# Kernel tuning notes

Measured on AMD Instinct MI355X. Metric: run time of the kernel, lower is better.

Reference implementation:

```python
import jax, jax.numpy as jnp
import numpy as np

B, A, C, H, S, NR = 128, 2048, 128, 512, 3, 2
PR = C + 3 + S   # 134 read params per head
PW = 3 * C + 3 + S  # 390 write params


def setup_inputs() -> dict:
    key = jax.random.key(0)
    ks = jax.random.split(key, 8)
    h = jax.random.normal(ks[0], (B, H), jnp.float32)
    mem = jax.random.normal(ks[1], (B, A, C), jnp.float32)
    ra = jax.random.uniform(ks[2], (NR, B, A), jnp.float32)
    ra = ra / ra.sum(-1, keepdims=True)  # valid attention distributions
    wa = jax.random.uniform(ks[3], (B, A), jnp.float32)
    wa = wa / wa.sum(-1, keepdims=True)
    W_read = 0.02 * jax.random.normal(ks[4], (NR, PR, H), jnp.float32)
    b_read = jnp.zeros((NR, PR), jnp.float32)
    W_write = 0.02 * jax.random.normal(ks[5], (PW, H), jnp.float32)
    b_write = jnp.zeros((PW,), jnp.float32)
    return dict(h=h, mem=mem, prev_read_attn=ra, prev_write_attn=wa,
                W_read=W_read, b_read=b_read, W_write=W_write, b_write=b_write)


def _addressing(query, beta, gate, shift, gamma, mem, prev_w):
    """NTM addressing. query [...,C] (raw), beta/gate/gamma [...,1], shift [...,S],
    mem [B,A,C] (broadcasts), prev_w [...,A]. Returns attention [...,A]."""
    eps = 1e-8
    q = jax.nn.sigmoid(query)
    beta = jax.nn.softplus(beta) + 1.0
    gate = jax.nn.sigmoid(gate)
    shift_w = jax.nn.softmax(shift, axis=-1)
    gamma = jax.nn.softplus(gamma) + 1.0
    # content-based addressing: cosine similarity + sharpened softmax over A
    qn = jnp.maximum(jnp.linalg.norm(q, axis=-1, keepdims=True), eps)      # [...,1]
    mn = jnp.maximum(jnp.linalg.norm(mem, axis=-1), eps)                   # [B,A]
    sim = jnp.einsum('...c,...ac->...a', q, mem) / (qn * mn)
    w_c = jax.nn.softmax(beta * sim, axis=-1)
    # gated interpolation with previous attention
    w_g = gate * w_c + (1.0 - gate) * prev_w
    # circular shift convolution, offsets -(S//2)..S//2
    K = S // 2
    idx = (jnp.arange(A)[:, None] - (jnp.arange(S)[None, :] - K)) % A      # [A,S]
    w_s = jnp.einsum('...as,...s->...a', w_g[..., idx], shift_w)
    # gamma sharpening
    w_pow = w_s ** gamma
    return w_pow / (w_pow.sum(-1, keepdims=True) + 1e-12)


def reference(h, mem, prev_read_attn, prev_write_attn, W_read, b_read, W_write, b_write):
    # --- read heads (vectorized over NR heads) ---
    pr = jnp.einsum('bh,rph->rbp', h, W_read) + b_read[:, None, :]         # [NR,B,PR]
    q, beta, gate, shift, gamma = jnp.split(pr, [C, C + 1, C + 2, C + 2 + S], axis=-1)
    read_w = _addressing(q, beta, gate, shift, gamma, mem, prev_read_attn)  # [NR,B,A]
    read_vectors = jnp.einsum('rba,bac->rbc', read_w, mem)                 # [NR,B,C]
    # --- write head ---
    pw = h @ W_write.T + b_write                                           # [B,PW]
    locs = np.cumsum([C, 1, 1, S, 1, C])
    qw, bw, gw, sw, gmw, erase, add = jnp.split(pw, locs.tolist(), axis=-1)
    write_w = _addressing(qw, bw, gw, sw, gmw, mem, prev_write_attn)       # [B,A]
    e = jax.nn.sigmoid(erase)[:, None, :]                                  # [B,1,C]
    a = jax.nn.sigmoid(add)[:, None, :]                                    # [B,1,C]
    w = write_w[..., None]                                                 # [B,A,1]
    new_mem = mem * (1.0 - w * e) + w * a
    return read_vectors, new_mem
```

## Files before the change

### kernel.cpp

```cpp
#include <hip/hip_runtime.h>
#include <math.h>

constexpr int B_  = 128;
constexpr int A_  = 2048;
constexpr int C_  = 128;
constexpr int H_  = 512;
constexpr int S_  = 3;
constexpr int NR_ = 2;
constexpr int PR_ = C_ + 3 + S_;
constexpr int PW_ = 3 * C_ + 3 + S_;

typedef float vfloat4 __attribute__((ext_vector_type(4)));

__device__ __forceinline__ float sigmoidf_(float x) { return 1.0f / (1.0f + expf(-x)); }
__device__ __forceinline__ float softplusf_(float x) {
  return fmaxf(x, 0.0f) + log1pf(expf(-fabsf(x)));
}

__device__ __forceinline__ float waveReduceSum(float v) {
#pragma unroll
  for (int off = 32; off; off >>= 1) v += __shfl_xor(v, off, 64);
  return v;
}
__device__ __forceinline__ float waveReduceMax(float v) {
#pragma unroll
  for (int off = 32; off; off >>= 1) v = fmaxf(v, __shfl_xor(v, off, 64));
  return v;
}

__device__ __forceinline__ float blockReduceSum(float v, float* rbuf) {
  int tid = threadIdx.x;
  v = waveReduceSum(v);
  if ((tid & 63) == 0) rbuf[tid >> 6] = v;
  __syncthreads();
  float r = rbuf[0] + rbuf[1] + rbuf[2] + rbuf[3];
  __syncthreads();
  return r;
}
__device__ __forceinline__ float blockReduceMax(float v, float* rbuf) {
  int tid = threadIdx.x;
  v = waveReduceMax(v);
  if ((tid & 63) == 0) rbuf[tid >> 6] = v;
  __syncthreads();
  float r = fmaxf(fmaxf(rbuf[0], rbuf[1]), fmaxf(rbuf[2], rbuf[3]));
  __syncthreads();
  return r;
}

__global__ __launch_bounds__(256) void proj_kernel(
    const float* __restrict__ h, const float* __restrict__ Wr,
    const float* __restrict__ br, const float* __restrict__ Ww,
    const float* __restrict__ bw, float* __restrict__ pr, float* __restrict__ pw) {
  constexpr int NPR = NR_ * B_ * PR_;
  constexpr int NPW = B_ * PW_;
  int wave = (blockIdx.x * blockDim.x + threadIdx.x) >> 6;
  int lane = threadIdx.x & 63;
  const float* wrow;
  const float* hrow;
  float bias;
  float* outp;
  if (wave < NPR) {
    int r = wave / (B_ * PR_);
    int rem = wave - r * (B_ * PR_);
    int b = rem / PR_;
    int p = rem - b * PR_;
    wrow = Wr + (size_t)(r * PR_ + p) * H_;
    hrow = h + (size_t)b * H_;
    bias = br[r * PR_ + p];
    outp = pr + wave;
  } else {
    int w2 = wave - NPR;
    if (w2 >= NPW) return;
    int b = w2 / PW_;
    int p = w2 - b * PW_;
    wrow = Ww + (size_t)p * H_;
    hrow = h + (size_t)b * H_;
    bias = bw[p];
    outp = pw + w2;
  }
  const float4* w4 = (const float4*)wrow;
  const float4* h4 = (const float4*)hrow;
  float4 a0 = h4[(lane << 1)];
  float4 a1 = h4[(lane << 1) + 1];
  float4 b0 = w4[(lane << 1)];
  float4 b1 = w4[(lane << 1) + 1];
  float acc = a0.x * b0.x;
  acc = fmaf(a0.y, b0.y, acc);
  acc = fmaf(a0.z, b0.z, acc);
  acc = fmaf(a0.w, b0.w, acc);
  acc = fmaf(a1.x, b1.x, acc);
  acc = fmaf(a1.y, b1.y, acc);
  acc = fmaf(a1.z, b1.z, acc);
  acc = fmaf(a1.w, b1.w, acc);
  acc = waveReduceSum(acc);
  if (lane == 0) *outp = acc + bias;
}

__global__ __launch_bounds__(64) void headprep_kernel(
    const float* __restrict__ pr, const float* __restrict__ pw,
    float* __restrict__ qbuf, float* __restrict__ qn, float* __restrict__ pars,
    float* __restrict__ rv) {
  int hb = blockIdx.x;
  int hd = hb >> 7;
  int b = hb & (B_ - 1);
  int lane = threadIdx.x;
  for (int i = hb * 64 + lane; i < NR_ * B_ * C_; i += 384 * 64) rv[i] = 0.0f;

  const float* src = (hd < 2) ? (pr + (size_t)hb * PR_) : (pw + (size_t)b * PW_);
  float2 raw = ((const float2*)src)[lane];
  float q0 = sigmoidf_(raw.x);
  float q1 = sigmoidf_(raw.y);
  ((float2*)(qbuf + (size_t)hb * C_))[lane] = make_float2(q0, q1);
  float ss = q0 * q0 + q1 * q1;
  ss = waveReduceSum(ss);
  if (lane == 0) {
    qn[hb] = fmaxf(sqrtf(ss), 1e-8f);
    float braw = src[C_];
    float graw = src[C_ + 1];
    float s0 = src[C_ + 2], s1 = src[C_ + 3], s2 = src[C_ + 4];
    float gmraw = src[C_ + 5];
    float mx = fmaxf(s0, fmaxf(s1, s2));
    float e0 = expf(s0 - mx), e1 = expf(s1 - mx), e2 = expf(s2 - mx);
    float inv = 1.0f / (e0 + e1 + e2);
    float* pp = pars + hb * 8;
    pp[0] = softplusf_(braw) + 1.0f;
    pp[1] = sigmoidf_(graw);
    pp[2] = e0 * inv;
    pp[3] = e1 * inv;
    pp[4] = e2 * inv;
    pp[5] = softplusf_(gmraw) + 1.0f;
  }
}

__global__ __launch_bounds__(256) void sim_kernel(
    const float* __restrict__ mem, const float* __restrict__ qbuf,
    const float* __restrict__ qn, float* __restrict__ sim) {
  __shared__ __align__(16) float qs[3 * C_];
  __shared__ float qnl[3];
  int b = blockIdx.x >> 5;
  int chunk = blockIdx.x & 31;
  int rowbase = chunk << 6;
  int tid = threadIdx.x;
  for (int idx = tid; idx < 3 * C_; idx += 256) {
    int hd = idx >> 7;
    int c = idx & (C_ - 1);
    qs[idx] = qbuf[(size_t)(hd * B_ + b) * C_ + c];
  }
  if (tid < 3) qnl[tid] = qn[tid * B_ + b];
  __syncthreads();

  int wv = tid >> 6;
  int lane = tid & 63;
  int j = lane & 7;
  int rsub = lane >> 3;

  float4 q0[4], q1[4], q2[4];
  const float4* qs4 = (const float4*)qs;
#pragma unroll
  for (int k = 0; k < 4; k++) {
    q0[k] = qs4[j + 8 * k];
    q1[k] = qs4[32 + j + 8 * k];
    q2[k] = qs4[64 + j + 8 * k];
  }
  float iqn0 = 1.0f / qnl[0], iqn1 = 1.0f / qnl[1], iqn2 = 1.0f / qnl[2];

#pragma unroll
  for (int it = 0; it < 2; it++) {
    int row = rowbase + (it << 5) + (wv << 3) + rsub;
    const float4* mrow = (const float4*)(mem + ((size_t)b * A_ + row) * C_);
    float d0 = 0.f, d1 = 0.f, d2 = 0.f, ss = 0.f;
#pragma unroll
    for (int k = 0; k < 4; k++) {
      float4 m = mrow[j + 8 * k];
      d0 = fmaf(m.x, q0[k].x, d0); d0 = fmaf(m.y, q0[k].y, d0);
      d0 = fmaf(m.z, q0[k].z, d0); d0 = fmaf(m.w, q0[k].w, d0);
      d1 = fmaf(m.x, q1[k].x, d1); d1 = fmaf(m.y, q1[k].y, d1);
      d1 = fmaf(m.z, q1[k].z, d1); d1 = fmaf(m.w, q1[k].w, d1);
      d2 = fmaf(m.x, q2[k].x, d2); d2 = fmaf(m.y, q2[k].y, d2);
      d2 = fmaf(m.z, q2[k].z, d2); d2 = fmaf(m.w, q2[k].w, d2);
      ss = fmaf(m.x, m.x, ss); ss = fmaf(m.y, m.y, ss);
      ss = fmaf(m.z, m.z, ss); ss = fmaf(m.w, m.w, ss);
    }
#pragma unroll
    for (int off = 1; off <= 4; off <<= 1) {
      d0 += __shfl_xor(d0, off, 64);
      d1 += __shfl_xor(d1, off, 64);
      d2 += __shfl_xor(d2, off, 64);
      ss += __shfl_xor(ss, off, 64);
    }
    if (j == 0) {
      float imn = 1.0f / fmaxf(sqrtf(ss), 1e-8f);
      sim[(size_t)(0 * B_ + b) * A_ + row] = d0 * iqn0 * imn;
      sim[(size_t)(1 * B_ + b) * A_ + row] = d1 * iqn1 * imn;
      sim[(size_t)(2 * B_ + b) * A_ + row] = d2 * iqn2 * imn;
    }
  }
}

__global__ __launch_bounds__(256) void attn_kernel(
    const float* __restrict__ sim, const float* __restrict__ ra,
    const float* __restrict__ wa, const float* __restrict__ pars,
    float* __restrict__ attn) {
  __shared__ float wg[A_];
  __shared__ float rbuf[4];
  int hb = blockIdx.x;
  int hd = hb >> 7;
  int b = hb & (B_ - 1);
  int tid = threadIdx.x;
  const float* pp = pars + hb * 8;
  float beta = pp[0], gate = pp[1], sw0 = pp[2], sw1 = pp[3], sw2 = pp[4], gamma = pp[5];
  const float* simrow = sim + (size_t)hb * A_;
  const float* prev = (hd < 2) ? (ra + (size_t)hb * A_) : (wa + (size_t)b * A_);
  float* outrow = attn + (size_t)hb * A_;

  float s[8];
  float mx = -1e30f;
#pragma unroll
  for (int i = 0; i < 8; i++) {
    s[i] = simrow[tid + (i << 8)];
    mx = fmaxf(mx, s[i]);
  }
  mx = blockReduceMax(mx, rbuf);
  float p[8];
  float lsum = 0.0f;
#pragma unroll
  for (int i = 0; i < 8; i++) {
    p[i] = expf(beta * (s[i] - mx));
    lsum += p[i];
  }
  float tot = blockReduceSum(lsum, rbuf);
  float inv = 1.0f / tot;
#pragma unroll
  for (int i = 0; i < 8; i++) {
    int a = tid + (i << 8);
    wg[a] = fmaf(gate, p[i] * inv, (1.0f - gate) * prev[a]);
  }
  __syncthreads();
  float lsum2 = 0.0f;
#pragma unroll
  for (int i = 0; i < 8; i++) {
    int a = tid + (i << 8);
    float ws = sw0 * wg[(a + 1) & (A_ - 1)] + sw1 * wg[a] + sw2 * wg[(a - 1) & (A_ - 1)];
    float wp = (ws > 0.0f) ? exp2f(gamma * log2f(ws)) : 0.0f;
    p[i] = wp;
    lsum2 += wp;
  }
  float tot2 = blockReduceSum(lsum2, rbuf);
  float inv2 = 1.0f / (tot2 + 1e-12f);
#pragma unroll
  for (int i = 0; i < 8; i++) {
    outrow[tid + (i << 8)] = p[i] * inv2;
  }
}

__global__ __launch_bounds__(256) void update_kernel(
    const float* __restrict__ mem, const float* __restrict__ attn,
    const float* __restrict__ pw, float* __restrict__ rv,
    float* __restrict__ nmem) {
  __shared__ float att0[256], att1[256], attw[256];
  __shared__ float4 red0[256];
  __shared__ float4 red1[256];
  int b = blockIdx.x >> 3;
  int chunk = blockIdx.x & 7;
  int rowbase = chunk << 8;
  int tid = threadIdx.x;
  att0[tid] = attn[(size_t)(0 * B_ + b) * A_ + rowbase + tid];
  att1[tid] = attn[(size_t)(1 * B_ + b) * A_ + rowbase + tid];
  attw[tid] = attn[(size_t)(2 * B_ + b) * A_ + rowbase + tid];
  __syncthreads();

  int rowlane = tid & 31;
  int rowoff = tid >> 5;
  int c0 = rowlane << 2;
  const float* pwrow = pw + (size_t)b * PW_;
  float2 eA = *(const float2*)(pwrow + C_ + 6 + c0);
  float2 eB = *(const float2*)(pwrow + C_ + 6 + c0 + 2);
  float2 aA = *(const float2*)(pwrow + 2 * C_ + 6 + c0);
  float2 aB = *(const float2*)(pwrow + 2 * C_ + 6 + c0 + 2);
  float e0 = sigmoidf_(eA.x), e1 = sigmoidf_(eA.y), e2 = sigmoidf_(eB.x), e3 = sigmoidf_(eB.y);
  float ad0 = sigmoidf_(aA.x), ad1 = sigmoidf_(aA.y), ad2 = sigmoidf_(aB.x), ad3 = sigmoidf_(aB.y);

  float4 acc0 = make_float4(0.f, 0.f, 0.f, 0.f);
  float4 acc1 = make_float4(0.f, 0.f, 0.f, 0.f);

#pragma unroll 4
  for (int i = 0; i < 32; i++) {
    int ridx = (i << 3) + rowoff;
    int row = rowbase + ridx;
    size_t base = ((size_t)b * A_ + row) * C_ + c0;
    float4 m = *(const float4*)(mem + base);
    float w0 = att0[ridx];
    float w1 = att1[ridx];
    float ww = attw[ridx];
    acc0.x = fmaf(w0, m.x, acc0.x);
    acc0.y = fmaf(w0, m.y, acc0.y);
    acc0.z = fmaf(w0, m.z, acc0.z);
    acc0.w = fmaf(w0, m.w, acc0.w);
    acc1.x = fmaf(w1, m.x, acc1.x);
    acc1.y = fmaf(w1, m.y, acc1.y);
    acc1.z = fmaf(w1, m.z, acc1.z);
    acc1.w = fmaf(w1, m.w, acc1.w);
    vfloat4 nm;
    nm.x = fmaf(m.x, 1.0f - ww * e0, ww * ad0);
    nm.y = fmaf(m.y, 1.0f - ww * e1, ww * ad1);
    nm.z = fmaf(m.z, 1.0f - ww * e2, ww * ad2);
    nm.w = fmaf(m.w, 1.0f - ww * e3, ww * ad3);
    __builtin_nontemporal_store(nm, (vfloat4*)(nmem + base));
  }

  red0[tid] = acc0;
  red1[tid] = acc1;
  __syncthreads();
#pragma unroll
  for (int s = 128; s >= 32; s >>= 1) {
    if (tid < s) {
      float4 x = red0[tid], y = red0[tid + s];
      x.x += y.x; x.y += y.y; x.z += y.z; x.w += y.w;
      red0[tid] = x;
      float4 u = red1[tid], v = red1[tid + s];
      u.x += v.x; u.y += v.y; u.z += v.z; u.w += v.w;
      red1[tid] = u;
    }
    __syncthreads();
  }
  if (tid < 32) {
    float4 r0 = red0[tid];
    float4 r1 = red1[tid];
    float* rv0 = rv + (size_t)(0 * B_ + b) * C_ + (tid << 2);
    float* rv1 = rv + (size_t)(1 * B_ + b) * C_ + (tid << 2);
    atomicAdd(rv0 + 0, r0.x);
    atomicAdd(rv0 + 1, r0.y);
    atomicAdd(rv0 + 2, r0.z);
    atomicAdd(rv0 + 3, r0.w);
    atomicAdd(rv1 + 0, r1.x);
    atomicAdd(rv1 + 1, r1.y);
    atomicAdd(rv1 + 2, r1.z);
    atomicAdd(rv1 + 3, r1.w);
  }
}

extern "C" void kernel_launch(void* const* d_in, const int* in_sizes, int n_in,
                              void* d_out, int out_size, void* d_ws, size_t ws_size,
                              hipStream_t stream) {
  const float* h   = (const float*)d_in[0];
  const float* mem = (const float*)d_in[1];
  const float* ra  = (const float*)d_in[2];
  const float* wa  = (const float*)d_in[3];
  const float* Wr  = (const float*)d_in[4];
  const float* br  = (const float*)d_in[5];
  const float* Ww  = (const float*)d_in[6];
  const float* bw  = (const float*)d_in[7];

  float* out = (float*)d_out;
  float* rv = out;
  float* nmem = out + NR_ * B_ * C_;

  float* ws = (float*)d_ws;
  float* pr_buf = ws;
  float* pw_buf = pr_buf + NR_ * B_ * PR_;
  float* qbuf   = pw_buf + B_ * PW_;
  float* qn     = qbuf + 3 * B_ * C_;
  float* pars   = qn + 3 * B_;
  float* simb   = pars + 3 * B_ * 8;

  constexpr int NWAVES = NR_ * B_ * PR_ + B_ * PW_;
  proj_kernel<<<dim3((NWAVES + 3) / 4), dim3(256), 0, stream>>>(h, Wr, br, Ww, bw, pr_buf, pw_buf);
  headprep_kernel<<<dim3(3 * B_), dim3(64), 0, stream>>>(pr_buf, pw_buf, qbuf, qn, pars, rv);
  sim_kernel<<<dim3(B_ * (A_ / 64)), dim3(256), 0, stream>>>(mem, qbuf, qn, simb);
  attn_kernel<<<dim3(3 * B_), dim3(256), 0, stream>>>(simb, ra, wa, pars, simb);
  update_kernel<<<dim3(B_ * (A_ / 256)), dim3(256), 0, stream>>>(mem, simb, pw_buf, rv, nmem);
}
```

Measured before the change: 291.3 us.

## Fold headprep into neighbors, pair projection rows, widen attn blocks, shuffle reductions

Removes the headprep kernel. Its sigmoid/norm work moves into sim_kernel, its scalar parameter transforms move into attn_kernel, and rv zeroing moves into proj_kernel. proj_kernel computes two outputs per wave so the h row load is shared. attn_kernel uses 1024-thread blocks with fewer reduction rounds, and update_kernel replaces the LDS tree reduction with a shuffle followed by a small LDS sum. The intent is to cut one launch and some sync overhead. The cost is that every sim block recomputes the sigmoid of q, and the pairing assumes the output counts are even and that row pairs stay within one head.

```diff
diff --git a/kernel.cpp b/kernel.cpp
--- a/kernel.cpp
+++ b/kernel.cpp
@@ -28,115 +28,84 @@
   return v;
 }
 
-__device__ __forceinline__ float blockReduceSum(float v, float* rbuf) {
-  int tid = threadIdx.x;
-  v = waveReduceSum(v);
-  if ((tid & 63) == 0) rbuf[tid >> 6] = v;
-  __syncthreads();
-  float r = rbuf[0] + rbuf[1] + rbuf[2] + rbuf[3];
-  __syncthreads();
-  return r;
-}
-__device__ __forceinline__ float blockReduceMax(float v, float* rbuf) {
-  int tid = threadIdx.x;
-  v = waveReduceMax(v);
-  if ((tid & 63) == 0) rbuf[tid >> 6] = v;
-  __syncthreads();
-  float r = fmaxf(fmaxf(rbuf[0], rbuf[1]), fmaxf(rbuf[2], rbuf[3]));
-  __syncthreads();
-  return r;
-}
-
 __global__ __launch_bounds__(256) void proj_kernel(
     const float* __restrict__ h, const float* __restrict__ Wr,
     const float* __restrict__ br, const float* __restrict__ Ww,
-    const float* __restrict__ bw, float* __restrict__ pr, float* __restrict__ pw) {
+    const float* __restrict__ bw, float* __restrict__ pr, float* __restrict__ pw,
+    float* __restrict__ rv) {
   constexpr int NPR = NR_ * B_ * PR_;
   constexpr int NPW = B_ * PW_;
-  int wave = (blockIdx.x * blockDim.x + threadIdx.x) >> 6;
+  int gid = blockIdx.x * 256 + threadIdx.x;
+  if (gid < NR_ * B_ * C_) rv[gid] = 0.0f;
+  int wave = gid >> 6;
   int lane = threadIdx.x & 63;
-  const float* wrow;
+  int out0 = wave * 2;
+  const float* w0row;
+  const float* w1row;
   const float* hrow;
-  float bias;
+  float bias0, bias1;
   float* outp;
-  if (wave < NPR) {
-    int r = wave / (B_ * PR_);
-    int rem = wave - r * (B_ * PR_);
+  if (out0 < NPR) {
+    int r = out0 / (B_ * PR_);
+    int rem = out0 - r * (B_ * PR_);
     int b = rem / PR_;
     int p = rem - b * PR_;
-    wrow = Wr + (size_t)(r * PR_ + p) * H_;
+    w0row = Wr + (size_t)(r * PR_ + p) * H_;
+    w1row = w0row + H_;
     hrow = h + (size_t)b * H_;
-    bias = br[r * PR_ + p];
-    outp = pr + wave;
+    bias0 = br[r * PR_ + p];
+    bias1 = br[r * PR_ + p + 1];
+    outp = pr + out0;
   } else {
-    int w2 = wave - NPR;
+    int w2 = out0 - NPR;
     if (w2 >= NPW) return;
     int b = w2 / PW_;
     int p = w2 - b * PW_;
-    wrow = Ww + (size_t)p * H_;
+    w0row = Ww + (size_t)p * H_;
+    w1row = w0row + H_;
     hrow = h + (size_t)b * H_;
-    bias = bw[p];
+    bias0 = bw[p];
+    bias1 = bw[p + 1];
     outp = pw + w2;
   }
-  const float4* w4 = (const float4*)wrow;
   const float4* h4 = (const float4*)hrow;
+  const float4* wa4 = (const float4*)w0row;
+  const float4* wb4 = (const float4*)w1row;
   float4 a0 = h4[(lane << 1)];
   float4 a1 = h4[(lane << 1) + 1];
-  float4 b0 = w4[(lane << 1)];
-  float4 b1 = w4[(lane << 1) + 1];
-  float acc = a0.x * b0.x;
-  acc = fmaf(a0.y, b0.y, acc);
-  acc = fmaf(a0.z, b0.z, acc);
-  acc = fmaf(a0.w, b0.w, acc);
-  acc = fmaf(a1.x, b1.x, acc);
-  acc = fmaf(a1.y, b1.y, acc);
-  acc = fmaf(a1.z, b1.z, acc);
-  acc = fmaf(a1.w, b1.w, acc);
-  acc = waveReduceSum(acc);
-  if (lane == 0) *outp = acc + bias;
-}
-
-__global__ __launch_bounds__(64) void headprep_kernel(
-    const float* __restrict__ pr, const float* __restrict__ pw,
-    float* __restrict__ qbuf, float* __restrict__ qn, float* __restrict__ pars,
-    float* __restrict__ rv) {
-  int hb = blockIdx.x;
-  int hd = hb >> 7;
-  int b = hb & (B_ - 1);
-  int lane = threadIdx.x;
-  for (int i = hb * 64 + lane; i < NR_ * B_ * C_; i += 384 * 64) rv[i] = 0.0f;
-
-  const float* src = (hd < 2) ? (pr + (size_t)hb * PR_) : (pw + (size_t)b * PW_);
-  float2 raw = ((const float2*)src)[lane];
-  float q0 = sigmoidf_(raw.x);
-  float q1 = sigmoidf_(raw.y);
-  ((float2*)(qbuf + (size_t)hb * C_))[lane] = make_float2(q0, q1);
-  float ss = q0 * q0 + q1 * q1;
-  ss = waveReduceSum(ss);
+  float4 b0 = wa4[(lane << 1)];
+  float4 b1 = wa4[(lane << 1) + 1];
+  float4 c0 = wb4[(lane << 1)];
+  float4 c1 = wb4[(lane << 1) + 1];
+  float acc0 = a0.x * b0.x;
+  acc0 = fmaf(a0.y, b0.y, acc0);
+  acc0 = fmaf(a0.z, b0.z, acc0);
+  acc0 = fmaf(a0.w, b0.w, acc0);
+  acc0 = fmaf(a1.x, b1.x, acc0);
+  acc0 = fmaf(a1.y, b1.y, acc0);
+  acc0 = fmaf(a1.z, b1.z, acc0);
+  acc0 = fmaf(a1.w, b1.w, acc0);
+  float acc1 = a0.x * c0.x;
+  acc1 = fmaf(a0.y, c0.y, acc1);
+  acc1 = fmaf(a0.z, c0.z, acc1);
+  acc1 = fmaf(a0.w, c0.w, acc1);
+  acc1 = fmaf(a1.x, c1.x, acc1);
+  acc1 = fmaf(a1.y, c1.y, acc1);
+  acc1 = fmaf(a1.z, c1.z, acc1);
+  acc1 = fmaf(a1.w, c1.w, acc1);
+  acc0 = waveReduceSum(acc0);
+  acc1 = waveReduceSum(acc1);
   if (lane == 0) {
-    qn[hb] = fmaxf(sqrtf(ss), 1e-8f);
-    float braw = src[C_];
-    float graw = src[C_ + 1];
-    float s0 = src[C_ + 2], s1 = src[C_ + 3], s2 = src[C_ + 4];
-    float gmraw = src[C_ + 5];
-    float mx = fmaxf(s0, fmaxf(s1, s2));
-    float e0 = expf(s0 - mx), e1 = expf(s1 - mx), e2 = expf(s2 - mx);
-    float inv = 1.0f / (e0 + e1 + e2);
-    float* pp = pars + hb * 8;
-    pp[0] = softplusf_(braw) + 1.0f;
-    pp[1] = sigmoidf_(graw);
-    pp[2] = e0 * inv;
-    pp[3] = e1 * inv;
-    pp[4] = e2 * inv;
-    pp[5] = softplusf_(gmraw) + 1.0f;
+    outp[0] = acc0 + bias0;
+    outp[1] = acc1 + bias1;
   }
 }
 
 __global__ __launch_bounds__(256) void sim_kernel(
-    const float* __restrict__ mem, const float* __restrict__ qbuf,
-    const float* __restrict__ qn, float* __restrict__ sim) {
+    const float* __restrict__ mem, const float* __restrict__ pr,
+    const float* __restrict__ pw, float* __restrict__ sim) {
   __shared__ __align__(16) float qs[3 * C_];
-  __shared__ float qnl[3];
+  __shared__ float iqn[3];
   int b = blockIdx.x >> 5;
   int chunk = blockIdx.x & 31;
   int rowbase = chunk << 6;
@@ -144,13 +113,22 @@
   for (int idx = tid; idx < 3 * C_; idx += 256) {
     int hd = idx >> 7;
     int c = idx & (C_ - 1);
-    qs[idx] = qbuf[(size_t)(hd * B_ + b) * C_ + c];
-  }
-  if (tid < 3) qnl[tid] = qn[tid * B_ + b];
-  __syncthreads();
-
+    float raw = (hd < 2) ? pr[(size_t)(hd * B_ + b) * PR_ + c]
+                         : pw[(size_t)b * PW_ + c];
+    qs[idx] = sigmoidf_(raw);
+  }
+  __syncthreads();
   int wv = tid >> 6;
   int lane = tid & 63;
+  if (wv < 3) {
+    float v0 = qs[wv * C_ + lane];
+    float v1 = qs[wv * C_ + 64 + lane];
+    float ss = v0 * v0 + v1 * v1;
+    ss = waveReduceSum(ss);
+    if (lane == 0) iqn[wv] = 1.0f / fmaxf(sqrtf(ss), 1e-8f);
+  }
+  __syncthreads();
+
   int j = lane & 7;
   int rsub = lane >> 3;
 
@@ -162,7 +140,7 @@
     q1[k] = qs4[32 + j + 8 * k];
     q2[k] = qs4[64 + j + 8 * k];
   }
-  float iqn0 = 1.0f / qnl[0], iqn1 = 1.0f / qnl[1], iqn2 = 1.0f / qnl[2];
+  float iqn0 = iqn[0], iqn1 = iqn[1], iqn2 = iqn[2];
 
 #pragma unroll
   for (int it = 0; it < 2; it++) {
@@ -197,60 +175,80 @@
   }
 }
 
-__global__ __launch_bounds__(256) void attn_kernel(
+__global__ __launch_bounds__(1024) void attn_kernel(
     const float* __restrict__ sim, const float* __restrict__ ra,
-    const float* __restrict__ wa, const float* __restrict__ pars,
-    float* __restrict__ attn) {
+    const float* __restrict__ wa, const float* __restrict__ pr,
+    const float* __restrict__ pw, float* __restrict__ attn) {
   __shared__ float wg[A_];
-  __shared__ float rbuf[4];
+  __shared__ float rb1[16], rb2[16], rb3[16];
   int hb = blockIdx.x;
   int hd = hb >> 7;
   int b = hb & (B_ - 1);
   int tid = threadIdx.x;
-  const float* pp = pars + hb * 8;
-  float beta = pp[0], gate = pp[1], sw0 = pp[2], sw1 = pp[3], sw2 = pp[4], gamma = pp[5];
+  int wv = tid >> 6;
+  int lane = tid & 63;
+  const float* src = (hd < 2) ? (pr + (size_t)hb * PR_) : (pw + (size_t)b * PW_);
+  float braw = src[C_];
+  float graw = src[C_ + 1];
+  float s0r = src[C_ + 2], s1r = src[C_ + 3], s2r = src[C_ + 4];
+  float gmraw = src[C_ + 5];
+  float mx3 = fmaxf(s0r, fmaxf(s1r, s2r));
+  float e0 = expf(s0r - mx3), e1 = expf(s1r - mx3), e2 = expf(s2r - mx3);
+  float sinv = 1.0f / (e0 + e1 + e2);
+  float beta = softplusf_(braw) + 1.0f;
+  float gate = sigmoidf_(graw);
+  float sw0 = e0 * sinv, sw1 = e1 * sinv, sw2 = e2 * sinv;
+  float gamma = softplusf_(gmraw) + 1.0f;
+
   const float* simrow = sim + (size_t)hb * A_;
   const float* prev = (hd < 2) ? (ra + (size_t)hb * A_) : (wa + (size_t)b * A_);
   float* outrow = attn + (size_t)hb * A_;
 
-  float s[8];
-  float mx = -1e30f;
-#pragma unroll
-  for (int i = 0; i < 8; i++) {
-    s[i] = simrow[tid + (i << 8)];
-    mx = fmaxf(mx, s[i]);
-  }
-  mx = blockReduceMax(mx, rbuf);
-  float p[8];
-  float lsum = 0.0f;
-#pragma unroll
-  for (int i = 0; i < 8; i++) {
-    p[i] = expf(beta * (s[i] - mx));
-    lsum += p[i];
-  }
-  float tot = blockReduceSum(lsum, rbuf);
-  float inv = 1.0f / tot;
-#pragma unroll
-  for (int i = 0; i < 8; i++) {
-    int a = tid + (i << 8);
-    wg[a] = fmaf(gate, p[i] * inv, (1.0f - gate) * prev[a]);
-  }
-  __syncthreads();
-  float lsum2 = 0.0f;
-#pragma unroll
-  for (int i = 0; i < 8; i++) {
-    int a = tid + (i << 8);
-    float ws = sw0 * wg[(a + 1) & (A_ - 1)] + sw1 * wg[a] + sw2 * wg[(a - 1) & (A_ - 1)];
-    float wp = (ws > 0.0f) ? exp2f(gamma * log2f(ws)) : 0.0f;
-    p[i] = wp;
-    lsum2 += wp;
-  }
-  float tot2 = blockReduceSum(lsum2, rbuf);
-  float inv2 = 1.0f / (tot2 + 1e-12f);
-#pragma unroll
-  for (int i = 0; i < 8; i++) {
-    outrow[tid + (i << 8)] = p[i] * inv2;
-  }
+  int a0 = tid;
+  int a1 = tid + 1024;
+  float s0 = simrow[a0];
+  float s1 = simrow[a1];
+  float pv0 = prev[a0];
+  float pv1 = prev[a1];
+
+  float mx = fmaxf(s0, s1);
+  mx = waveReduceMax(mx);
+  if (lane == 0) rb1[wv] = mx;
+  __syncthreads();
+  float M = rb1[0];
+#pragma unroll
+  for (int i = 1; i < 16; i++) M = fmaxf(M, rb1[i]);
+
+  float p0 = expf(beta * (s0 - M));
+  float p1 = expf(beta * (s1 - M));
+  float l = p0 + p1;
+  l = waveReduceSum(l);
+  if (lane == 0) rb2[wv] = l;
+  __syncthreads();
+  float T = rb2[0];
+#pragma unroll
+  for (int i = 1; i < 16; i++) T += rb2[i];
+  float inv = 1.0f / T;
+
+  wg[a0] = fmaf(gate, p0 * inv, (1.0f - gate) * pv0);
+  wg[a1] = fmaf(gate, p1 * inv, (1.0f - gate) * pv1);
+  __syncthreads();
+
+  float ws0 = sw0 * wg[(a0 + 1) & (A_ - 1)] + sw1 * wg[a0] + sw2 * wg[(a0 - 1) & (A_ - 1)];
+  float ws1 = sw0 * wg[(a1 + 1) & (A_ - 1)] + sw1 * wg[a1] + sw2 * wg[(a1 - 1) & (A_ - 1)];
+  float wp0 = (ws0 > 0.0f) ? exp2f(gamma * log2f(ws0)) : 0.0f;
+  float wp1 = (ws1 > 0.0f) ? exp2f(gamma * log2f(ws1)) : 0.0f;
+  float l2 = wp0 + wp1;
+  l2 = waveReduceSum(l2);
+  if (lane == 0) rb3[wv] = l2;
+  __syncthreads();
+  float T2 = rb3[0];
+#pragma unroll
+  for (int i = 1; i < 16; i++) T2 += rb3[i];
+  float inv2 = 1.0f / (T2 + 1e-12f);
+
+  outrow[a0] = wp0 * inv2;
+  outrow[a1] = wp1 * inv2;
 }
 
 __global__ __launch_bounds__(256) void update_kernel(
@@ -258,8 +256,8 @@
     const float* __restrict__ pw, float* __restrict__ rv,
     float* __restrict__ nmem) {
   __shared__ float att0[256], att1[256], attw[256];
-  __shared__ float4 red0[256];
-  __shared__ float4 red1[256];
+  __shared__ float4 red0[128];
+  __shared__ float4 red1[128];
   int b = blockIdx.x >> 3;
   int chunk = blockIdx.x & 7;
   int rowbase = chunk << 8;
@@ -308,24 +306,31 @@
     __builtin_nontemporal_store(nm, (vfloat4*)(nmem + base));
   }
 
-  red0[tid] = acc0;
-  red1[tid] = acc1;
-  __syncthreads();
-#pragma unroll
-  for (int s = 128; s >= 32; s >>= 1) {
-    if (tid < s) {
-      float4 x = red0[tid], y = red0[tid + s];
-      x.x += y.x; x.y += y.y; x.z += y.z; x.w += y.w;
-      red0[tid] = x;
-      float4 u = red1[tid], v = red1[tid + s];
-      u.x += v.x; u.y += v.y; u.z += v.z; u.w += v.w;
-      red1[tid] = u;
-    }
-    __syncthreads();
-  }
+  int lane = tid & 63;
+  int wv = tid >> 6;
+  acc0.x += __shfl_xor(acc0.x, 32, 64);
+  acc0.y += __shfl_xor(acc0.y, 32, 64);
+  acc0.z += __shfl_xor(acc0.z, 32, 64);
+  acc0.w += __shfl_xor(acc0.w, 32, 64);
+  acc1.x += __shfl_xor(acc1.x, 32, 64);
+  acc1.y += __shfl_xor(acc1.y, 32, 64);
+  acc1.z += __shfl_xor(acc1.z, 32, 64);
+  acc1.w += __shfl_xor(acc1.w, 32, 64);
+  if (lane < 32) {
+    red0[wv * 32 + lane] = acc0;
+    red1[wv * 32 + lane] = acc1;
+  }
+  __syncthreads();
   if (tid < 32) {
     float4 r0 = red0[tid];
+    float4 t;
+    t = red0[tid + 32]; r0.x += t.x; r0.y += t.y; r0.z += t.z; r0.w += t.w;
+    t = red0[tid + 64]; r0.x += t.x; r0.y += t.y; r0.z += t.z; r0.w += t.w;
+    t = red0[tid + 96]; r0.x += t.x; r0.y += t.y; r0.z += t.z; r0.w += t.w;
     float4 r1 = red1[tid];
+    t = red1[tid + 32]; r1.x += t.x; r1.y += t.y; r1.z += t.z; r1.w += t.w;
+    t = red1[tid + 64]; r1.x += t.x; r1.y += t.y; r1.z += t.z; r1.w += t.w;
+    t = red1[tid + 96]; r1.x += t.x; r1.y += t.y; r1.z += t.z; r1.w += t.w;
     float* rv0 = rv + (size_t)(0 * B_ + b) * C_ + (tid << 2);
     float* rv1 = rv + (size_t)(1 * B_ + b) * C_ + (tid << 2);
     atomicAdd(rv0 + 0, r0.x);
@@ -358,15 +363,11 @@
   float* ws = (float*)d_ws;
   float* pr_buf = ws;
   float* pw_buf = pr_buf + NR_ * B_ * PR_;
-  float* qbuf   = pw_buf + B_ * PW_;
-  float* qn     = qbuf + 3 * B_ * C_;
-  float* pars   = qn + 3 * B_;
-  float* simb   = pars + 3 * B_ * 8;
-
-  constexpr int NWAVES = NR_ * B_ * PR_ + B_ * PW_;
-  proj_kernel<<<dim3((NWAVES + 3) / 4), dim3(256), 0, stream>>>(h, Wr, br, Ww, bw, pr_buf, pw_buf);
-  headprep_kernel<<<dim3(3 * B_), dim3(64), 0, stream>>>(pr_buf, pw_buf, qbuf, qn, pars, rv);
-  sim_kernel<<<dim3(B_ * (A_ / 64)), dim3(256), 0, stream>>>(mem, qbuf, qn, simb);
-  attn_kernel<<<dim3(3 * B_), dim3(256), 0, stream>>>(simb, ra, wa, pars, simb);
+  float* simb   = pw_buf + B_ * PW_;
+
+  constexpr int NPAIRS = (NR_ * B_ * PR_ + B_ * PW_) / 2;
+  proj_kernel<<<dim3(NPAIRS / 4), dim3(256), 0, stream>>>(h, Wr, br, Ww, bw, pr_buf, pw_buf, rv);
+  sim_kernel<<<dim3(B_ * (A_ / 64)), dim3(256), 0, stream>>>(mem, pr_buf, pw_buf, simb);
+  attn_kernel<<<dim3(3 * B_), dim3(1024), 0, stream>>>(simb, ra, wa, pr_buf, pw_buf, simb);
   update_kernel<<<dim3(B_ * (A_ / 256)), dim3(256), 0, stream>>>(mem, simb, pw_buf, rv, nmem);
 }
```

New measurement: 289.1 us (median of 2 runs). About the same (-0.8%).
